# Kernel tuning notes

Measured on AMD Instinct MI355X. Metric: run time of the kernel, lower is better.

## Reference

```python
import jax, jax.numpy as jnp
import numpy as np

SIGMA = 10.0


def setup_inputs() -> dict:
    key = jax.random.key(0)
    k1, k2 = jax.random.split(key)
    B, C, K, D = 1024, 1000, 4, 1024
    f = jax.random.normal(k1, (B, D), dtype=jnp.float32)
    # kaiming_normal_ on (C, K, D): fan_in = K*D, std = sqrt(2/fan_in)
    std = np.sqrt(2.0 / (K * D)).astype(np.float32)
    centers = jax.random.normal(k2, (C, K, D), dtype=jnp.float32) * std
    return {"f": f, "centers": centers}


def reference(f, centers):
    B, D = f.shape
    C, K, _ = centers.shape
    mc = C * K
    w = centers.reshape(mc, D)  # [mc, D]

    # ||f - w||^2 = |f|^2 + |w|^2 - 2 f.w  (avoids [B,C,K,D] broadcast tensor)
    f_sq = jnp.sum(f * f, axis=-1, keepdims=True)            # [B, 1]
    w_sq = jnp.sum(w * w, axis=-1)                           # [mc]
    fw = f @ w.T                                             # [B, mc] GEMM
    fw_norm = jnp.maximum(f_sq + w_sq[None, :] - 2.0 * fw, 0.0)
    distance = jnp.exp(-fw_norm / SIGMA).reshape(B, C, K)
    distance = jnp.max(distance, axis=-1)                    # [B, C]

    # pairwise center regularization
    ww = w @ w.T                                             # [mc, mc]
    w_norm_mat = jnp.maximum(w_sq[:, None] + w_sq[None, :] - 2.0 * ww, 0.0)
    w_norm_upper = jnp.triu(w_norm_mat)
    denom = 2.0 / (mc * mc - mc)
    mu = denom * jnp.sum(w_norm_upper)
    residuals = jnp.triu((w_norm_upper - mu) ** 2)
    rw = denom * jnp.sum(residuals)

    rw_broadcast = jnp.ones((B, 1), dtype=f.dtype) * rw
    return jnp.concatenate((distance, rw_broadcast), axis=-1)  # [B, C+1]
```

## Files before the change

kernel.cpp:

```cpp
#include <hip/hip_runtime.h>

#define BB 1024
#define CC 1000
#define DD 1024
#define MC 4000
#define MCP 4096
#define SIGMA_INV (1.0f/10.0f)

typedef __attribute__((ext_vector_type(8))) short bf16x8;
typedef __attribute__((ext_vector_type(4))) float f32x4;

#define GLDS16(g, l) __builtin_amdgcn_global_load_lds( \
    (const __attribute__((address_space(1))) void*)(g), \
    (__attribute__((address_space(3))) void*)(l), 16, 0, 0)

__device__ __forceinline__ unsigned short f2bf(float x) {
  unsigned u = __float_as_uint(x);
  unsigned r = (u + 0x7fffu + ((u >> 16) & 1u)) >> 16;
  return (unsigned short)r;
}

__global__ __launch_bounds__(256) void prep_kernel(
    const float* __restrict__ f, const float* __restrict__ centers,
    unsigned short* __restrict__ fbf, unsigned short* __restrict__ wbf,
    float* __restrict__ f_sq, float* __restrict__ w_sq,
    double* __restrict__ acc2)
{
  if (blockIdx.x == 0 && threadIdx.x == 0) { acc2[0] = 0.0; acc2[1] = 0.0; }
  const int wv = threadIdx.x >> 6, lane = threadIdx.x & 63;
  const int row = blockIdx.x * 4 + wv;
  const float* src = nullptr;
  unsigned short* dst;
  float* sqp;
  if (row < BB) {
    src = f + (size_t)row * DD; dst = fbf + (size_t)row * DD; sqp = f_sq + row;
  } else {
    int wr = row - BB;
    dst = wbf + (size_t)wr * DD; sqp = w_sq + wr;
    if (wr < MC) src = centers + (size_t)wr * DD;
  }
  float ssum = 0.f;
#pragma unroll
  for (int p = 0; p < 4; ++p) {
    int idx = p * 256 + lane * 4;
    float4 v = make_float4(0.f, 0.f, 0.f, 0.f);
    if (src) v = *(const float4*)(src + idx);
    ssum += v.x * v.x + v.y * v.y + v.z * v.z + v.w * v.w;
    ushort4 o;
    o.x = f2bf(v.x); o.y = f2bf(v.y); o.z = f2bf(v.z); o.w = f2bf(v.w);
    *(ushort4*)(dst + idx) = o;
  }
#pragma unroll
  for (int s = 32; s; s >>= 1) ssum += __shfl_xor(ssum, s);
  if (lane == 0) *sqp = ssum;
}

__device__ __forceinline__ void stage_tile(
    const unsigned short* __restrict__ gbase, size_t row0, int k0,
    unsigned short* lds, int tid)
{
#pragma unroll
  for (int i = 0; i < 4; ++i) {
    int idx = i * 256 + tid;
    int drow = idx >> 3, dslot = idx & 7;
    int schunk = dslot ^ (drow & 7);
    GLDS16(gbase + (row0 + (size_t)drow) * DD + k0 + schunk * 8, &lds[idx * 8]);
  }
}

__global__ __launch_bounds__(256, 3) void gemm_kernel(
    const unsigned short* __restrict__ fbf, const unsigned short* __restrict__ wbf,
    const float* __restrict__ f_sq, const float* __restrict__ w_sq,
    float* __restrict__ out, double* __restrict__ acc2)
{
  __shared__ __align__(16) unsigned short As[128 * 64];
  __shared__ __align__(16) unsigned short Bs[128 * 64];
  __shared__ double rbuf[8];

  const int orig = blockIdx.x;
  const int bid = (orig & 7) * 98 + (orig >> 3);
  const bool is_fw = bid < 256;
  int tr, tc;
  const unsigned short* Abase;
  if (is_fw) {
    tr = bid >> 5; tc = bid & 31;
    Abase = fbf;
  } else {
    int t = bid - 256;
    tr = 0;
    while (t >= 32 - tr) { t -= 32 - tr; ++tr; }
    tc = tr + t;
    Abase = wbf;
  }

  const int tid = threadIdx.x;
  const int lane = tid & 63, wv = tid >> 6;
  const int wr = wv >> 1, wc = wv & 1;
  const int rlo = lane & 15, rhi = lane >> 4, rx = lane & 7;

  f32x4 acc[4][4] = {};

  for (int kt = 0; kt < DD / 64; ++kt) {
    stage_tile(Abase, (size_t)tr * 128, kt * 64, As, tid);
    stage_tile(wbf,  (size_t)tc * 128, kt * 64, Bs, tid);
    __syncthreads();
#pragma unroll
    for (int kk = 0; kk < 2; ++kk) {
      bf16x8 af[4], bw[4];
#pragma unroll
      for (int m = 0; m < 4; ++m) {
        int row = wr * 64 + m * 16 + rlo;
        int slot = (kk * 4 + rhi) ^ rx;
        af[m] = *(const bf16x8*)&As[row * 64 + slot * 8];
      }
#pragma unroll
      for (int n = 0; n < 4; ++n) {
        int row = wc * 64 + n * 16 + rlo;
        int slot = (kk * 4 + rhi) ^ rx;
        bw[n] = *(const bf16x8*)&Bs[row * 64 + slot * 8];
      }
#pragma unroll
      for (int m = 0; m < 4; ++m)
#pragma unroll
        for (int n = 0; n < 4; ++n)
          acc[m][n] = __builtin_amdgcn_mfma_f32_16x16x32_bf16(af[m], bw[n], acc[m][n], 0, 0, 0);
    }
    __syncthreads();
  }

  if (is_fw) {
#pragma unroll
    for (int m = 0; m < 4; ++m) {
      int row = tr * 128 + wr * 64 + m * 16 + rhi * 4;
#pragma unroll
      for (int n = 0; n < 4; ++n) {
        int col = tc * 128 + wc * 64 + n * 16 + rlo;
        float wsq = w_sq[col];
#pragma unroll
        for (int r = 0; r < 4; ++r) {
          float fn = f_sq[row + r] + wsq - 2.0f * acc[m][n][r];
          fn = fmaxf(fn, 0.f);
          float dist = __expf(-fn * SIGMA_INV);
          dist = fmaxf(dist, __shfl_xor(dist, 1));
          dist = fmaxf(dist, __shfl_xor(dist, 2));
          if ((lane & 3) == 0 && col < MC)
            out[(size_t)(row + r) * (CC + 1) + (col >> 2)] = dist;
        }
      }
    }
  } else {
    double s1 = 0.0, s2 = 0.0;
#pragma unroll
    for (int m = 0; m < 4; ++m) {
      int i0 = tr * 128 + wr * 64 + m * 16 + rhi * 4;
#pragma unroll
      for (int n = 0; n < 4; ++n) {
        int j = tc * 128 + wc * 64 + n * 16 + rlo;
        float wsqj = (j < MC) ? w_sq[j] : 0.f;
#pragma unroll
        for (int r = 0; r < 4; ++r) {
          int i = i0 + r;
          if (i < MC && j < MC && j >= i) {
            float s = fmaxf(w_sq[i] + wsqj - 2.0f * acc[m][n][r], 0.f);
            s1 += (double)s;
            double d = (double)s - 1.0;
            s2 += d * d;
          }
        }
      }
    }
#pragma unroll
    for (int s = 32; s; s >>= 1) { s1 += __shfl_xor(s1, s); s2 += __shfl_xor(s2, s); }
    if (lane == 0) { rbuf[wv * 2] = s1; rbuf[wv * 2 + 1] = s2; }
    __syncthreads();
    if (tid == 0) {
      atomicAdd(&acc2[0], rbuf[0] + rbuf[2] + rbuf[4] + rbuf[6]);
      atomicAdd(&acc2[1], rbuf[1] + rbuf[3] + rbuf[5] + rbuf[7]);
    }
  }
}

__global__ __launch_bounds__(256) void finalize_kernel(
    const double* __restrict__ acc2, float* __restrict__ out)
{
  __shared__ float rws;
  if (threadIdx.x == 0) {
    double SS1 = acc2[0], SS2 = acc2[1];
    double denom = 2.0 / ((double)MC * (double)MC - (double)MC);
    double mu = denom * SS1;
    double T = (double)MC * (double)(MC + 1) * 0.5;
    double sm1 = SS1 - T;
    double dm = mu - 1.0;
    double resid = SS2 - 2.0 * dm * sm1 + T * dm * dm;
    rws = (float)(denom * resid);
  }
  __syncthreads();
  float v = rws;
  for (int b = threadIdx.x; b < BB; b += 256)
    out[(size_t)b * (CC + 1) + CC] = v;
}

extern "C" void kernel_launch(void* const* d_in, const int* in_sizes, int n_in,
                              void* d_out, int out_size, void* d_ws, size_t ws_size,
                              hipStream_t stream) {
  const float* f = (const float*)d_in[0];
  const float* centers = (const float*)d_in[1];
  float* out = (float*)d_out;
  char* ws = (char*)d_ws;

  double* acc2        = (double*)(ws + 0);
  float* f_sq         = (float*)(ws + 4096);
  float* w_sq         = (float*)(ws + 8192);
  unsigned short* fbf = (unsigned short*)(ws + 24576);
  unsigned short* wbf = (unsigned short*)(ws + 24576 + 2 * 1024 * 1024);

  prep_kernel<<<(BB + MCP) / 4, 256, 0, stream>>>(f, centers, fbf, wbf, f_sq, w_sq, acc2);
  gemm_kernel<<<784, 256, 0, stream>>>(fbf, wbf, f_sq, w_sq, out, acc2);
  finalize_kernel<<<1, 256, 0, stream>>>(acc2, out);
}
```

Before: 114.1 us.

## Use 256x256 tiles with 8 waves and double-buffered ping-pong MFMA pipeline

Replaces the 128x128 tile, single-buffered GEMM with 256x256 tiles computed by 512-thread blocks (8 waves). Global-to-LDS loads are double-buffered and interleaved with MFMA quarters, using explicit barriers, sched_barrier and setprio to overlap loads with compute. The aim is to raise arithmetic intensity and hide memory latency. In exchange the grid shrinks from 784 to 200 blocks on a 256-CU part, which adds tail and wave-quantization imbalance, and LDS use grows to 128KB per block.

```diff
diff --git a/kernel.cpp b/kernel.cpp
--- a/kernel.cpp
+++ b/kernel.cpp
@@ -6,6 +6,8 @@
 #define MC 4000
 #define MCP 4096
 #define SIGMA_INV (1.0f/10.0f)
+#define NT 16
+#define NIT 8
 
 typedef __attribute__((ext_vector_type(8))) short bf16x8;
 typedef __attribute__((ext_vector_type(4))) float f32x4;
@@ -13,6 +15,10 @@
 #define GLDS16(g, l) __builtin_amdgcn_global_load_lds( \
     (const __attribute__((address_space(1))) void*)(g), \
     (__attribute__((address_space(3))) void*)(l), 16, 0, 0)
+
+#define SBAR()   __builtin_amdgcn_s_barrier()
+#define SCHED()  __builtin_amdgcn_sched_barrier(0)
+#define PRIO(x)  __builtin_amdgcn_s_setprio(x)
 
 __device__ __forceinline__ unsigned short f2bf(float x) {
   unsigned u = __float_as_uint(x);
@@ -55,90 +61,152 @@
   if (lane == 0) *sqp = ssum;
 }
 
-__device__ __forceinline__ void stage_tile(
-    const unsigned short* __restrict__ gbase, size_t row0, int k0,
-    unsigned short* lds, int tid)
-{
-#pragma unroll
-  for (int i = 0; i < 4; ++i) {
-    int idx = i * 256 + tid;
-    int drow = idx >> 3, dslot = idx & 7;
-    int schunk = dslot ^ (drow & 7);
-    GLDS16(gbase + (row0 + (size_t)drow) * DD + k0 + schunk * 8, &lds[idx * 8]);
-  }
-}
-
-__global__ __launch_bounds__(256, 3) void gemm_kernel(
+
+#define STAGE(SET, AB, SRC, K0, H) do { \
+  GLDS16((SRC) + (K0) + soff[(H)*2+0], &lds[SET][AB][doff[(H)*2+0]]); \
+  GLDS16((SRC) + (K0) + soff[(H)*2+1], &lds[SET][AB][doff[(H)*2+1]]); \
+} while(0)
+
+#define READ_A(SET, MH) do { \
+  _Pragma("unroll") for (int ks = 0; ks < 2; ++ks) \
+  _Pragma("unroll") for (int m = 0; m < 4; ++m) { \
+    int row = wr*128 + ((MH)*4 + m)*16 + rlo; \
+    int slot = (ks*4 + rhi) ^ rx; \
+    af[ks][m] = *(const bf16x8*)&lds[SET][0][row*64 + slot*8]; \
+  } } while(0)
+
+#define READ_B(SET, NH, BW) do { \
+  _Pragma("unroll") for (int ks = 0; ks < 2; ++ks) \
+  _Pragma("unroll") for (int n = 0; n < 2; ++n) { \
+    int row = wc*64 + ((NH)*2 + n)*16 + rlo; \
+    int slot = (ks*4 + rhi) ^ rx; \
+    BW[ks][n] = *(const bf16x8*)&lds[SET][1][row*64 + slot*8]; \
+  } } while(0)
+
+#define MFMA_Q(MH, NH, BW) do { \
+  _Pragma("unroll") for (int ks = 0; ks < 2; ++ks) \
+  _Pragma("unroll") for (int m = 0; m < 4; ++m) \
+  _Pragma("unroll") for (int n = 0; n < 2; ++n) \
+    acc[(MH)*4+m][(NH)*2+n] = __builtin_amdgcn_mfma_f32_16x16x32_bf16( \
+        af[ks][m], BW[ks][n], acc[(MH)*4+m][(NH)*2+n], 0, 0, 0); \
+} while(0)
+
+#define PHASE_MID() do { SCHED(); SBAR(); SCHED(); PRIO(1); } while(0)
+#define PHASE_END() do { PRIO(0); SCHED(); SBAR(); SCHED(); } while(0)
+
+__global__ __launch_bounds__(512, 2) void gemm_kernel(
     const unsigned short* __restrict__ fbf, const unsigned short* __restrict__ wbf,
     const float* __restrict__ f_sq, const float* __restrict__ w_sq,
     float* __restrict__ out, double* __restrict__ acc2)
 {
-  __shared__ __align__(16) unsigned short As[128 * 64];
-  __shared__ __align__(16) unsigned short Bs[128 * 64];
-  __shared__ double rbuf[8];
+  __shared__ __align__(16) unsigned short lds[2][2][256 * 64];
+
+  const int tid = threadIdx.x;
+  const int lane = tid & 63, wv = tid >> 6;
+  const int wr = wv >> 2, wc = wv & 3;
+  const int rlo = lane & 15, rhi = lane >> 4, rx = lane & 7;
 
   const int orig = blockIdx.x;
-  const int bid = (orig & 7) * 98 + (orig >> 3);
-  const bool is_fw = bid < 256;
+  const int bid = (orig & 7) * 25 + (orig >> 3);
+  const bool is_fw = bid < 64;
   int tr, tc;
   const unsigned short* Abase;
   if (is_fw) {
-    tr = bid >> 5; tc = bid & 31;
+    tr = bid >> 4; tc = bid & 15;
     Abase = fbf;
   } else {
-    int t = bid - 256;
+    int t = bid - 64;
     tr = 0;
-    while (t >= 32 - tr) { t -= 32 - tr; ++tr; }
+    while (t >= 16 - tr) { t -= 16 - tr; ++tr; }
     tc = tr + t;
     Abase = wbf;
   }
-
-  const int tid = threadIdx.x;
-  const int lane = tid & 63, wv = tid >> 6;
-  const int wr = wv >> 1, wc = wv & 1;
-  const int rlo = lane & 15, rhi = lane >> 4, rx = lane & 7;
-
-  f32x4 acc[4][4] = {};
-
-  for (int kt = 0; kt < DD / 64; ++kt) {
-    stage_tile(Abase, (size_t)tr * 128, kt * 64, As, tid);
-    stage_tile(wbf,  (size_t)tc * 128, kt * 64, Bs, tid);
-    __syncthreads();
-#pragma unroll
-    for (int kk = 0; kk < 2; ++kk) {
-      bf16x8 af[4], bw[4];
-#pragma unroll
-      for (int m = 0; m < 4; ++m) {
-        int row = wr * 64 + m * 16 + rlo;
-        int slot = (kk * 4 + rhi) ^ rx;
-        af[m] = *(const bf16x8*)&As[row * 64 + slot * 8];
-      }
-#pragma unroll
-      for (int n = 0; n < 4; ++n) {
-        int row = wc * 64 + n * 16 + rlo;
-        int slot = (kk * 4 + rhi) ^ rx;
-        bw[n] = *(const bf16x8*)&Bs[row * 64 + slot * 8];
-      }
-#pragma unroll
-      for (int m = 0; m < 4; ++m)
-#pragma unroll
-        for (int n = 0; n < 4; ++n)
-          acc[m][n] = __builtin_amdgcn_mfma_f32_16x16x32_bf16(af[m], bw[n], acc[m][n], 0, 0, 0);
-    }
-    __syncthreads();
+  const unsigned short* Arow = Abase + (size_t)tr * 256 * DD;
+  const unsigned short* Brow = wbf  + (size_t)tc * 256 * DD;
+
+  int soff[4], doff[4];
+#pragma unroll
+  for (int h = 0; h < 2; ++h)
+#pragma unroll
+    for (int i = 0; i < 2; ++i) {
+      int idx = h * 1024 + i * 512 + tid;
+      int drow = idx >> 3, dslot = idx & 7;
+      int schunk = dslot ^ (drow & 7);
+      soff[h * 2 + i] = drow * DD + schunk * 8;
+      doff[h * 2 + i] = idx * 8;
+    }
+
+  f32x4 acc[8][4] = {};
+  bf16x8 af[2][4], bw0[2][2], bw1[2][2];
+
+  STAGE(0, 0, Arow, 0, 0);
+  STAGE(0, 0, Arow, 0, 1);
+  STAGE(0, 1, Brow, 0, 0);
+  STAGE(0, 1, Brow, 0, 1);
+  STAGE(1, 1, Brow, 64, 0);
+  STAGE(1, 1, Brow, 64, 1);
+  SCHED();
+  asm volatile("s_waitcnt vmcnt(4)" ::: "memory");
+  SCHED();
+  SBAR();
+  SCHED();
+
+#pragma unroll 1
+  for (int it = 0; it < NIT; ++it) {
+    const int ka  = (2 * it + 1) * 64;
+    const int kb0 = (2 * it + 2) * 64;
+    const int kb1 = (2 * it + 3) * 64;
+    const bool st = (it < NIT - 1);
+
+    READ_A(0, 0); READ_B(0, 0, bw0);
+    STAGE(1, 0, Arow, ka, 0);
+    PHASE_MID(); MFMA_Q(0, 0, bw0); PHASE_END();
+
+    READ_B(0, 1, bw1);
+    STAGE(1, 0, Arow, ka, 1);
+    PHASE_MID(); MFMA_Q(0, 1, bw1); PHASE_END();
+
+    READ_A(0, 1);
+    if (st) STAGE(0, 1, Brow, kb0, 0);
+    PHASE_MID(); MFMA_Q(1, 1, bw1); PHASE_END();
+
+    if (st) STAGE(0, 1, Brow, kb0, 1);
+    PHASE_MID(); MFMA_Q(1, 0, bw0);
+    PRIO(0); SCHED();
+    if (st) asm volatile("s_waitcnt vmcnt(4)" ::: "memory");
+    else    asm volatile("s_waitcnt vmcnt(0)" ::: "memory");
+    SCHED(); SBAR(); SCHED();
+
+    READ_A(1, 0); READ_B(1, 0, bw0);
+    if (st) STAGE(0, 0, Arow, kb0, 0);
+    PHASE_MID(); MFMA_Q(0, 0, bw0); PHASE_END();
+
+    READ_B(1, 1, bw1);
+    if (st) STAGE(0, 0, Arow, kb0, 1);
+    PHASE_MID(); MFMA_Q(0, 1, bw1); PHASE_END();
+
+    READ_A(1, 1);
+    if (st) STAGE(1, 1, Brow, kb1, 0);
+    PHASE_MID(); MFMA_Q(1, 1, bw1); PHASE_END();
+
+    if (st) STAGE(1, 1, Brow, kb1, 1);
+    PHASE_MID(); MFMA_Q(1, 0, bw0);
+    PRIO(0); SCHED();
+    asm volatile("s_waitcnt vmcnt(4)" ::: "memory");
+    SCHED(); SBAR(); SCHED();
   }
 
   if (is_fw) {
 #pragma unroll
-    for (int m = 0; m < 4; ++m) {
-      int row = tr * 128 + wr * 64 + m * 16 + rhi * 4;
-#pragma unroll
-      for (int n = 0; n < 4; ++n) {
-        int col = tc * 128 + wc * 64 + n * 16 + rlo;
+    for (int mf = 0; mf < 8; ++mf) {
+      int row = tr * 256 + wr * 128 + mf * 16 + rhi * 4;
+#pragma unroll
+      for (int nf = 0; nf < 4; ++nf) {
+        int col = tc * 256 + wc * 64 + nf * 16 + rlo;
         float wsq = w_sq[col];
 #pragma unroll
         for (int r = 0; r < 4; ++r) {
-          float fn = f_sq[row + r] + wsq - 2.0f * acc[m][n][r];
+          float fn = f_sq[row + r] + wsq - 2.0f * acc[mf][nf][r];
           fn = fmaxf(fn, 0.f);
           float dist = __expf(-fn * SIGMA_INV);
           dist = fmaxf(dist, __shfl_xor(dist, 1));
@@ -151,17 +219,17 @@
   } else {
     double s1 = 0.0, s2 = 0.0;
 #pragma unroll
-    for (int m = 0; m < 4; ++m) {
-      int i0 = tr * 128 + wr * 64 + m * 16 + rhi * 4;
-#pragma unroll
-      for (int n = 0; n < 4; ++n) {
-        int j = tc * 128 + wc * 64 + n * 16 + rlo;
+    for (int mf = 0; mf < 8; ++mf) {
+      int i0 = tr * 256 + wr * 128 + mf * 16 + rhi * 4;
+#pragma unroll
+      for (int nf = 0; nf < 4; ++nf) {
+        int j = tc * 256 + wc * 64 + nf * 16 + rlo;
         float wsqj = (j < MC) ? w_sq[j] : 0.f;
 #pragma unroll
         for (int r = 0; r < 4; ++r) {
           int i = i0 + r;
           if (i < MC && j < MC && j >= i) {
-            float s = fmaxf(w_sq[i] + wsqj - 2.0f * acc[m][n][r], 0.f);
+            float s = fmaxf(w_sq[i] + wsqj - 2.0f * acc[mf][nf][r], 0.f);
             s1 += (double)s;
             double d = (double)s - 1.0;
             s2 += d * d;
@@ -171,11 +239,15 @@
     }
 #pragma unroll
     for (int s = 32; s; s >>= 1) { s1 += __shfl_xor(s1, s); s2 += __shfl_xor(s2, s); }
-    if (lane == 0) { rbuf[wv * 2] = s1; rbuf[wv * 2 + 1] = s2; }
+    double* rbuf = (double*)&lds[0][0][0];
+    if (lane == 0) { rbuf[wv] = s1; rbuf[8 + wv] = s2; }
     __syncthreads();
     if (tid == 0) {
-      atomicAdd(&acc2[0], rbuf[0] + rbuf[2] + rbuf[4] + rbuf[6]);
-      atomicAdd(&acc2[1], rbuf[1] + rbuf[3] + rbuf[5] + rbuf[7]);
+      double t1 = 0.0, t2 = 0.0;
+#pragma unroll
+      for (int w = 0; w < 8; ++w) { t1 += rbuf[w]; t2 += rbuf[8 + w]; }
+      atomicAdd(&acc2[0], t1);
+      atomicAdd(&acc2[1], t2);
     }
   }
 }
@@ -215,6 +287,6 @@
   unsigned short* wbf = (unsigned short*)(ws + 24576 + 2 * 1024 * 1024);
 
   prep_kernel<<<(BB + MCP) / 4, 256, 0, stream>>>(f, centers, fbf, wbf, f_sq, w_sq, acc2);
-  gemm_kernel<<<784, 256, 0, stream>>>(fbf, wbf, f_sq, w_sq, out, acc2);
+  gemm_kernel<<<200, 512, 0, stream>>>(fbf, wbf, f_sq, w_sq, out, acc2);
   finalize_kernel<<<1, 256, 0, stream>>>(acc2, out);
 }
```

After: 117.0 us. +2.5%, slower.
